# Performance work log

Hardware: AMD Instinct MI355X
Metric: run time of the kernel (lower is better)

The kernel has to match this reference:

```python
import jax, jax.numpy as jnp
import numpy as np
import math

# ---------------- irreps configuration (mul, l, parity) ----------------
MUL = 32
IRREPS_IN1 = [(MUL, 0, 1), (MUL, 1, -1), (MUL, 2, 1)]   # 32x0e + 32x1o + 32x2e
IRREPS_IN2 = [(1, 0, 1), (1, 1, -1), (1, 2, 1)]          # 1x0e + 1x1o + 1x2e (edge spherical harmonics)
IRREPS_OUT = [(MUL, 0, 1), (MUL, 1, -1), (MUL, 2, 1)]
BATCH = 8192

def _dim(irreps):
    return sum(mul * (2 * l + 1) for mul, l, _ in irreps)

# ---------------- real Wigner-3j tensors (e3nn convention) ----------------
def _su2_cg_coeff(j1, m1, j2, m2, j3, m3):
    if m3 != m1 + m2:
        return 0.0
    f = math.factorial
    vmin = max(-j1 + j2 + m3, -j1 + m1, 0)
    vmax = min(j2 + j3 + m1, j3 - j1 + j2, j3 + m3)
    C = math.sqrt((2 * j3 + 1) * f(j3 + j1 - j2) * f(j3 - j1 + j2) * f(j1 + j2 - j3)
                  * f(j3 + m3) * f(j3 - m3)
                  / (f(j1 + j2 + j3 + 1) * f(j1 - m1) * f(j1 + m1) * f(j2 - m2) * f(j2 + m2)))
    S = 0.0
    for v in range(vmin, vmax + 1):
        S += (-1.0) ** (v + j2 + m2) * f(j2 + j3 + m1 - v) * f(j1 - m1 + v) / (
            f(v) * f(j3 - j1 + j2 - v) * f(j3 + m3 - v) * f(v + j1 - j2 - m3))
    return C * S

def _su2_cg(l1, l2, l3):
    m = np.zeros((2 * l1 + 1, 2 * l2 + 1, 2 * l3 + 1))
    for m1 in range(-l1, l1 + 1):
        for m2 in range(-l2, l2 + 1):
            m3 = m1 + m2
            if abs(m3) <= l3:
                m[l1 + m1, l2 + m2, l3 + m3] = _su2_cg_coeff(l1, m1, l2, m2, l3, m3)
    return m / math.sqrt(2 * l3 + 1)  # 3j normalization -> Frobenius norm 1

def _q(l):
    # change of basis real -> complex spherical harmonics, with (-i)^l phase to make 3j real
    q = np.zeros((2 * l + 1, 2 * l + 1), dtype=np.complex128)
    for m in range(-l, 0):
        q[l + m, l + abs(m)] = 1 / math.sqrt(2)
        q[l + m, l - abs(m)] = -1j / math.sqrt(2)
    q[l, l] = 1.0
    for m in range(1, l + 1):
        q[l + m, l + abs(m)] = (-1) ** m / math.sqrt(2)
        q[l + m, l - abs(m)] = 1j * (-1) ** m / math.sqrt(2)
    return (-1j) ** l * q

def _w3j(l1, l2, l3):
    Ccplx = _su2_cg(l1, l2, l3).astype(np.complex128)
    Q1, Q2, Q3 = _q(l1), _q(l2), _q(l3)
    C = np.einsum('ij,kl,mn,ikm->jln', Q1, Q2, np.conj(Q3), Ccplx)
    if np.abs(C.imag).max() > 1e-8:  # robust fallback for basis-direction convention
        C = np.einsum('ji,lk,nm,ikm->jln', np.conj(Q1), np.conj(Q2), Q3, Ccplx)
    return np.real(C).astype(np.float32)

W3J = {}
for _m1, l1, _p1 in IRREPS_IN1:
    for _m2, l2, _p2 in IRREPS_IN2:
        for l3 in range(abs(l1 - l2), l1 + l2 + 1):
            if (l1, l2, l3) not in W3J:
                W3J[(l1, l2, l3)] = _w3j(l1, l2, l3)

# ---------------- tp output structure and linear weight layout ----------------
def _tp_irreps_out():
    irr = []
    for mul1, l1, p1 in IRREPS_IN1:
        for mul2, l2, p2 in IRREPS_IN2:
            for l3 in range(abs(l1 - l2), l1 + l2 + 1):
                irr.append((mul1 * mul2, l3, p1 * p2))
    return irr

TP_IRREPS = _tp_irreps_out()
WEIGHT_NUMEL = sum(mul_out * sum(m for m, li, pi in TP_IRREPS if (li, pi) == (l, p))
                   for mul_out, l, p in IRREPS_OUT)  # = 11264

# ---------------- forward ----------------
def _full_tp(x, y):
    # x: [B, 288], y: [B, 9] -> z: [B, 2592], 15 CG paths, 'uvuv' mode, component norm
    segs = []
    off1 = 0
    for mul1, l1, p1 in IRREPS_IN1:
        d1 = 2 * l1 + 1
        x1 = x[:, off1:off1 + mul1 * d1].reshape(-1, mul1, d1)
        off1 += mul1 * d1
        off2 = 0
        for mul2, l2, p2 in IRREPS_IN2:
            d2 = 2 * l2 + 1
            x2 = y[:, off2:off2 + mul2 * d2].reshape(-1, mul2, d2)
            off2 += mul2 * d2
            for l3 in range(abs(l1 - l2), l1 + l2 + 1):
                C = jnp.asarray(W3J[(l1, l2, l3)])
                z = jnp.einsum('ijk,bui,bvj->buvk', C, x1, x2) * np.float32(math.sqrt(2 * l3 + 1))
                segs.append(z.reshape(z.shape[0], -1))
    return jnp.concatenate(segs, axis=1)

def _linear(z, weight):
    # e3nn o3.Linear with external per-sample weights, element path normalization
    zsegs, off = [], 0
    for mul, l, p in TP_IRREPS:
        d = 2 * l + 1
        zsegs.append((z[:, off:off + mul * d].reshape(-1, mul, d), l, p))
        off += mul * d
    outs, woff = [], 0
    for mul_out, l, p in IRREPS_OUT:
        xin = jnp.concatenate([s for s, li, pi in zsegs if (li, pi) == (l, p)], axis=1)  # [B, U, d]
        U = xin.shape[1]
        w = weight[:, woff:woff + U * mul_out].reshape(-1, U, mul_out)
        woff += U * mul_out
        o = jnp.einsum('bud,buo->bod', xin, w) * np.float32(1.0 / math.sqrt(U))
        outs.append(o.reshape(o.shape[0], -1))
    return jnp.concatenate(outs, axis=1)

def setup_inputs() -> dict:
    key = jax.random.key(0)
    k1, k2, k3 = jax.random.split(key, 3)
    x = jax.random.normal(k1, (BATCH, _dim(IRREPS_IN1)), dtype=jnp.float32)
    y = jax.random.normal(k2, (BATCH, _dim(IRREPS_IN2)), dtype=jnp.float32)
    weight = jax.random.normal(k3, (BATCH, WEIGHT_NUMEL), dtype=jnp.float32)
    return {"x": x, "y": y, "weight": weight}

def reference(x, y, weight):
    z = _full_tp(x, y)
    return _linear(z, weight)
```

## Files before the change

### kernel.cpp

```cpp
#include <hip/hip_runtime.h>


using f4 = float __attribute__((ext_vector_type(4)));

__device__ inline f4 wred8(f4 v) {
#pragma unroll
    for (int m = 8; m <= 32; m <<= 1) {
        v.x += __shfl_xor(v.x, m);
        v.y += __shfl_xor(v.y, m);
        v.z += __shfl_xor(v.z, m);
        v.w += __shfl_xor(v.w, m);
    }
    return v;
}

__global__ __launch_bounds__(256) void etp_fused(
    const float* __restrict__ xg,
    const float* __restrict__ yg,
    const float* __restrict__ wg,
    float* __restrict__ outg)
{
    const int b = blockIdx.x;
    const int t = threadIdx.x;

    __shared__ __align__(16) float xs[288];
    __shared__ float ys[9];
    __shared__ float z0s[96];
    __shared__ float z1s[384];
    __shared__ float z2s[640];
    __shared__ float red[288 * 5];

    if (t < 72) {
        reinterpret_cast<f4*>(xs)[t] =
            __builtin_nontemporal_load(reinterpret_cast<const f4*>(xg) + (size_t)b * 72 + t);
    } else if (t < 81) {
        ys[t - 72] = yg[(size_t)b * 9 + (t - 72)];
    }

    const int oq = t & 7;
    const int ug = t >> 3;
    const f4* w4 = reinterpret_cast<const f4*>(wg) + (size_t)b * 2816;

    f4 wa0 = __builtin_nontemporal_load(&w4[(0 * 32 + ug) * 8 + oq]);
    f4 wa1 = __builtin_nontemporal_load(&w4[(1 * 32 + ug) * 8 + oq]);
    f4 wa2 = __builtin_nontemporal_load(&w4[(2 * 32 + ug) * 8 + oq]);
    f4 wb0 = __builtin_nontemporal_load(&w4[768 + (0 * 32 + ug) * 8 + oq]);
    f4 wb1 = __builtin_nontemporal_load(&w4[768 + (1 * 32 + ug) * 8 + oq]);
    f4 wb2 = __builtin_nontemporal_load(&w4[768 + (2 * 32 + ug) * 8 + oq]);
    f4 wb3 = __builtin_nontemporal_load(&w4[768 + (3 * 32 + ug) * 8 + oq]);
    f4 wc0 = __builtin_nontemporal_load(&w4[1792 + (0 * 32 + ug) * 8 + oq]);
    f4 wc1 = __builtin_nontemporal_load(&w4[1792 + (1 * 32 + ug) * 8 + oq]);
    f4 wc2 = __builtin_nontemporal_load(&w4[1792 + (2 * 32 + ug) * 8 + oq]);
    f4 wc3 = __builtin_nontemporal_load(&w4[1792 + (3 * 32 + ug) * 8 + oq]);

    __syncthreads();

    const float y0 = ys[0];
    const float ya = ys[1], yb = ys[2], yc = ys[3];
    const float Y0 = ys[4], Y1 = ys[5], Y2 = ys[6], Y3 = ys[7], Y4 = ys[8];

    constexpr float S3  = 0.5477225575051661f;
    constexpr float D3  = 0.31622776601683794f;
    constexpr float TD3 = 0.6324555320336759f;
    constexpr float S5  = 0.7071067811865476f;
    constexpr float D5  = 0.4082482904638631f;
    constexpr float P5  = 0.5345224838248488f;
    constexpr float Q5  = 0.2672612419124244f;
    constexpr float R5  = 0.4629100498862757f;
    constexpr float N3  = 0.5773502691896258f;
    constexpr float N5  = 0.4472135954999579f;

    if (t < 128) {
        const int u = t;
        float o0, o1, o2;
        if (u < 32) {
            const float s = xs[u];
            o0 = s * ya; o1 = s * yb; o2 = s * yc;
        } else if (u < 64) {
            const float* p = &xs[32 + 3 * (u - 32)];
            o0 = p[0] * y0; o1 = p[1] * y0; o2 = p[2] * y0;
        } else if (u < 96) {
            const float* p = &xs[32 + 3 * (u - 64)];
            const float a = p[0], bz = p[1], cx = p[2];
            o0 = S3 * (cx * Y0 + bz * Y1 - a * Y4) - D3 * a * Y2;
            o1 = S3 * (a * Y1 + cx * Y3) + TD3 * bz * Y2;
            o2 = S3 * (a * Y0 + bz * Y3 + cx * Y4) - D3 * cx * Y2;
        } else {
            const float* p = &xs[128 + 5 * (u - 96)];
            const float X0 = p[0], X1 = p[1], X2 = p[2], X3 = p[3], X4 = p[4];
            o0 = S3 * (yc * X0 + yb * X1 - ya * X4) - D3 * ya * X2;
            o1 = S3 * (ya * X1 + yc * X3) + TD3 * yb * X2;
            o2 = S3 * (ya * X0 + yb * X3 + yc * X4) - D3 * yc * X2;
        }
        z1s[3 * u] = o0; z1s[3 * u + 1] = o1; z1s[3 * u + 2] = o2;
    } else {
        const int u = t - 128;
        float c0, c1, c2, c3, c4;
        if (u < 32) {
            const float s = xs[u];
            c0 = s * Y0; c1 = s * Y1; c2 = s * Y2; c3 = s * Y3; c4 = s * Y4;
        } else if (u < 64) {
            const float* p = &xs[32 + 3 * (u - 32)];
            const float a = p[0], bz = p[1], cx = p[2];
            c0 = S5 * (a * yc + cx * ya);
            c1 = S5 * (a * yb + bz * ya);
            c2 = D5 * (2.0f * bz * yb - a * ya - cx * yc);
            c3 = S5 * (cx * yb + bz * yc);
            c4 = S5 * (cx * yc - a * ya);
        } else if (u < 96) {
            const float* p = &xs[128 + 5 * (u - 64)];
            c0 = p[0] * y0; c1 = p[1] * y0; c2 = p[2] * y0; c3 = p[3] * y0; c4 = p[4] * y0;
        } else {
            const float* p = &xs[128 + 5 * (u - 96)];
            const float X0 = p[0], X1 = p[1], X2 = p[2], X3 = p[3], X4 = p[4];
            c0 = -P5 * (X0 * Y2 + X2 * Y0) + R5 * (X1 * Y3 + X3 * Y1);
            c1 =  Q5 * (X1 * Y2 + X2 * Y1) - R5 * (X1 * Y4 + X4 * Y1) + R5 * (X0 * Y3 + X3 * Y0);
            c2 =  P5 * (X2 * Y2 - X0 * Y0 - X4 * Y4) + Q5 * (X1 * Y1 + X3 * Y3);
            c3 =  Q5 * (X3 * Y2 + X2 * Y3) + R5 * (X3 * Y4 + X4 * Y3) + R5 * (X0 * Y1 + X1 * Y0);
            c4 = -P5 * (X4 * Y2 + X2 * Y4) + R5 * (X3 * Y3 - X1 * Y1);
        }
        float* zp = &z2s[5 * u];
        zp[0] = c0; zp[1] = c1; zp[2] = c2; zp[3] = c3; zp[4] = c4;
    }
    if (t < 96) {
        float v;
        if (t < 32) {
            v = xs[t] * y0;
        } else if (t < 64) {
            const float* p = &xs[32 + 3 * (t - 32)];
            v = N3 * (p[0] * ya + p[1] * yb + p[2] * yc);
        } else {
            const float* p = &xs[128 + 5 * (t - 64)];
            v = N5 * (p[0] * Y0 + p[1] * Y1 + p[2] * Y2 + p[3] * Y3 + p[4] * Y4);
        }
        z0s[t] = v;
    }
    __syncthreads();

    f4 a0   = wa0 * z0s[ug] + wa1 * z0s[32 + ug] + wa2 * z0s[64 + ug];

    f4 a1k0 = {0,0,0,0}, a1k1 = {0,0,0,0}, a1k2 = {0,0,0,0};
    {
        const f4 w0 = wb0, w1 = wb1, w2 = wb2, w3 = wb3;
        const int u0 = ug, u1 = 32 + ug, u2 = 64 + ug, u3 = 96 + ug;
        a1k0 = w0 * z1s[3*u0]   + w1 * z1s[3*u1]   + w2 * z1s[3*u2]   + w3 * z1s[3*u3];
        a1k1 = w0 * z1s[3*u0+1] + w1 * z1s[3*u1+1] + w2 * z1s[3*u2+1] + w3 * z1s[3*u3+1];
        a1k2 = w0 * z1s[3*u0+2] + w1 * z1s[3*u1+2] + w2 * z1s[3*u2+2] + w3 * z1s[3*u3+2];
    }
    f4 a2k0, a2k1, a2k2, a2k3, a2k4;
    {
        const f4 w0 = wc0, w1 = wc1, w2 = wc2, w3 = wc3;
        const int u0 = ug, u1 = 32 + ug, u2 = 64 + ug, u3 = 96 + ug;
        a2k0 = w0 * z2s[5*u0]   + w1 * z2s[5*u1]   + w2 * z2s[5*u2]   + w3 * z2s[5*u3];
        a2k1 = w0 * z2s[5*u0+1] + w1 * z2s[5*u1+1] + w2 * z2s[5*u2+1] + w3 * z2s[5*u3+1];
        a2k2 = w0 * z2s[5*u0+2] + w1 * z2s[5*u1+2] + w2 * z2s[5*u2+2] + w3 * z2s[5*u3+2];
        a2k3 = w0 * z2s[5*u0+3] + w1 * z2s[5*u1+3] + w2 * z2s[5*u2+3] + w3 * z2s[5*u3+3];
        a2k4 = w0 * z2s[5*u0+4] + w1 * z2s[5*u1+4] + w2 * z2s[5*u2+4] + w3 * z2s[5*u3+4];
    }

    a0   = wred8(a0);
    a1k0 = wred8(a1k0); a1k1 = wred8(a1k1); a1k2 = wred8(a1k2);
    a2k0 = wred8(a2k0); a2k1 = wred8(a2k1); a2k2 = wred8(a2k2);
    a2k3 = wred8(a2k3); a2k4 = wred8(a2k4);

    const int lane = t & 63;
    const int wv   = t >> 6;
    if ((lane >> 3) == 0) {
        const int o = lane * 4;
#pragma unroll
        for (int j = 0; j < 4; ++j) {
            red[(o + j) * 5 + wv]                       = a0[j];
            red[(32 + (o + j) * 3 + 0) * 5 + wv]        = a1k0[j];
            red[(32 + (o + j) * 3 + 1) * 5 + wv]        = a1k1[j];
            red[(32 + (o + j) * 3 + 2) * 5 + wv]        = a1k2[j];
            red[(128 + (o + j) * 5 + 0) * 5 + wv]       = a2k0[j];
            red[(128 + (o + j) * 5 + 1) * 5 + wv]       = a2k1[j];
            red[(128 + (o + j) * 5 + 2) * 5 + wv]       = a2k2[j];
            red[(128 + (o + j) * 5 + 3) * 5 + wv]       = a2k3[j];
            red[(128 + (o + j) * 5 + 4) * 5 + wv]       = a2k4[j];
        }
    }
    __syncthreads();

    if (t < 72) {
        const float scale = (t < 8) ? 0.10206207261596575f
                                    : 0.08838834764831845f;
        f4 r;
#pragma unroll
        for (int j = 0; j < 4; ++j) {
            const int idx = 4 * t + j;
            r[j] = (red[idx * 5 + 0] + red[idx * 5 + 1] +
                    red[idx * 5 + 2] + red[idx * 5 + 3]) * scale;
        }
        __builtin_nontemporal_store(r, reinterpret_cast<f4*>(outg) + (size_t)b * 72 + t);
    }
}

extern "C" void kernel_launch(void* const* d_in, const int* in_sizes, int n_in,
                              void* d_out, int out_size, void* d_ws, size_t ws_size,
                              hipStream_t stream) {
    const float* x = (const float*)d_in[0];
    const float* y = (const float*)d_in[1];
    const float* w = (const float*)d_in[2];
    float* out = (float*)d_out;
    const int rows = in_sizes[0] / 288;
    etp_fused<<<rows, 256, 0, stream>>>(x, y, w, out);
}
```

Baseline: 65.10 us.

## Process four rows per block with register prefetch of next row's inputs

Each block now loops over four consecutive batch rows instead of one. It issues the next row's x, y and weight loads into registers right after the current row's weights have been consumed, so global memory latency overlaps with the contraction and reduction work. The grid shrinks by four, which cuts block launch and setup overhead. In exchange there are fewer resident blocks to hide latency, each iteration serializes more barriers, and register pressure rises.

After: 74.46 us. 14.4% more time.

```diff
diff --git a/kernel.cpp b/kernel.cpp
--- a/kernel.cpp
+++ b/kernel.cpp
@@ -2,6 +2,8 @@
 
 
 using f4 = float __attribute__((ext_vector_type(4)));
+
+#define ROWS 4
 
 __device__ inline f4 wred8(f4 v) {
 #pragma unroll
@@ -18,10 +20,11 @@
     const float* __restrict__ xg,
     const float* __restrict__ yg,
     const float* __restrict__ wg,
-    float* __restrict__ outg)
+    float* __restrict__ outg,
+    int nrows)
 {
-    const int b = blockIdx.x;
     const int t = threadIdx.x;
+    const int row0 = blockIdx.x * ROWS;
 
     __shared__ __align__(16) float xs[288];
     __shared__ float ys[9];
@@ -30,34 +33,46 @@
     __shared__ float z2s[640];
     __shared__ float red[288 * 5];
 
-    if (t < 72) {
-        reinterpret_cast<f4*>(xs)[t] =
-            __builtin_nontemporal_load(reinterpret_cast<const f4*>(xg) + (size_t)b * 72 + t);
-    } else if (t < 81) {
-        ys[t - 72] = yg[(size_t)b * 9 + (t - 72)];
-    }
-
     const int oq = t & 7;
     const int ug = t >> 3;
-    const f4* w4 = reinterpret_cast<const f4*>(wg) + (size_t)b * 2816;
-
-    f4 wa0 = __builtin_nontemporal_load(&w4[(0 * 32 + ug) * 8 + oq]);
-    f4 wa1 = __builtin_nontemporal_load(&w4[(1 * 32 + ug) * 8 + oq]);
-    f4 wa2 = __builtin_nontemporal_load(&w4[(2 * 32 + ug) * 8 + oq]);
-    f4 wb0 = __builtin_nontemporal_load(&w4[768 + (0 * 32 + ug) * 8 + oq]);
-    f4 wb1 = __builtin_nontemporal_load(&w4[768 + (1 * 32 + ug) * 8 + oq]);
-    f4 wb2 = __builtin_nontemporal_load(&w4[768 + (2 * 32 + ug) * 8 + oq]);
-    f4 wb3 = __builtin_nontemporal_load(&w4[768 + (3 * 32 + ug) * 8 + oq]);
-    f4 wc0 = __builtin_nontemporal_load(&w4[1792 + (0 * 32 + ug) * 8 + oq]);
-    f4 wc1 = __builtin_nontemporal_load(&w4[1792 + (1 * 32 + ug) * 8 + oq]);
-    f4 wc2 = __builtin_nontemporal_load(&w4[1792 + (2 * 32 + ug) * 8 + oq]);
-    f4 wc3 = __builtin_nontemporal_load(&w4[1792 + (3 * 32 + ug) * 8 + oq]);
-
-    __syncthreads();
-
-    const float y0 = ys[0];
-    const float ya = ys[1], yb = ys[2], yc = ys[3];
-    const float Y0 = ys[4], Y1 = ys[5], Y2 = ys[6], Y3 = ys[7], Y4 = ys[8];
+    const f4* xg4 = reinterpret_cast<const f4*>(xg);
+
+    f4 xv = {0, 0, 0, 0};
+    float yv = 0.f;
+    f4 wa0, wa1, wa2, wb0, wb1, wb2, wb3, wc0, wc1, wc2, wc3;
+
+    auto issue_xy = [&](int r) {
+        if (t < 72) {
+            xv = __builtin_nontemporal_load(&xg4[(size_t)r * 72 + t]);
+        } else if (t < 81) {
+            yv = yg[(size_t)r * 9 + (t - 72)];
+        }
+    };
+    auto issue_wa = [&](int r) {
+        const f4* w4 = reinterpret_cast<const f4*>(wg) + (size_t)r * 2816;
+        wa0 = __builtin_nontemporal_load(&w4[(0 * 32 + ug) * 8 + oq]);
+        wa1 = __builtin_nontemporal_load(&w4[(1 * 32 + ug) * 8 + oq]);
+        wa2 = __builtin_nontemporal_load(&w4[(2 * 32 + ug) * 8 + oq]);
+    };
+    auto issue_wb = [&](int r) {
+        const f4* w4 = reinterpret_cast<const f4*>(wg) + (size_t)r * 2816;
+        wb0 = __builtin_nontemporal_load(&w4[768 + (0 * 32 + ug) * 8 + oq]);
+        wb1 = __builtin_nontemporal_load(&w4[768 + (1 * 32 + ug) * 8 + oq]);
+        wb2 = __builtin_nontemporal_load(&w4[768 + (2 * 32 + ug) * 8 + oq]);
+        wb3 = __builtin_nontemporal_load(&w4[768 + (3 * 32 + ug) * 8 + oq]);
+    };
+    auto issue_wc = [&](int r) {
+        const f4* w4 = reinterpret_cast<const f4*>(wg) + (size_t)r * 2816;
+        wc0 = __builtin_nontemporal_load(&w4[1792 + (0 * 32 + ug) * 8 + oq]);
+        wc1 = __builtin_nontemporal_load(&w4[1792 + (1 * 32 + ug) * 8 + oq]);
+        wc2 = __builtin_nontemporal_load(&w4[1792 + (2 * 32 + ug) * 8 + oq]);
+        wc3 = __builtin_nontemporal_load(&w4[1792 + (3 * 32 + ug) * 8 + oq]);
+    };
+
+    issue_xy(row0);
+    issue_wa(row0);
+    issue_wb(row0);
+    issue_wc(row0);
 
     constexpr float S3  = 0.5477225575051661f;
     constexpr float D3  = 0.31622776601683794f;
@@ -70,129 +85,156 @@
     constexpr float N3  = 0.5773502691896258f;
     constexpr float N5  = 0.4472135954999579f;
 
-    if (t < 128) {
-        const int u = t;
-        float o0, o1, o2;
-        if (u < 32) {
-            const float s = xs[u];
-            o0 = s * ya; o1 = s * yb; o2 = s * yc;
-        } else if (u < 64) {
-            const float* p = &xs[32 + 3 * (u - 32)];
-            o0 = p[0] * y0; o1 = p[1] * y0; o2 = p[2] * y0;
-        } else if (u < 96) {
-            const float* p = &xs[32 + 3 * (u - 64)];
-            const float a = p[0], bz = p[1], cx = p[2];
-            o0 = S3 * (cx * Y0 + bz * Y1 - a * Y4) - D3 * a * Y2;
-            o1 = S3 * (a * Y1 + cx * Y3) + TD3 * bz * Y2;
-            o2 = S3 * (a * Y0 + bz * Y3 + cx * Y4) - D3 * cx * Y2;
+    for (int rr = 0; rr < ROWS; ++rr) {
+        const int r = row0 + rr;
+        if (r >= nrows) break;
+        const bool more = (rr + 1 < ROWS) && (r + 1 < nrows);
+
+        if (t < 72) {
+            reinterpret_cast<f4*>(xs)[t] = xv;
+        } else if (t < 81) {
+            ys[t - 72] = yv;
+        }
+        __syncthreads();
+
+        const float y0 = ys[0];
+        const float ya = ys[1], yb = ys[2], yc = ys[3];
+        const float Y0 = ys[4], Y1 = ys[5], Y2 = ys[6], Y3 = ys[7], Y4 = ys[8];
+
+        if (t < 128) {
+            const int u = t;
+            float o0, o1, o2;
+            if (u < 32) {
+                const float s = xs[u];
+                o0 = s * ya; o1 = s * yb; o2 = s * yc;
+            } else if (u < 64) {
+                const float* p = &xs[32 + 3 * (u - 32)];
+                o0 = p[0] * y0; o1 = p[1] * y0; o2 = p[2] * y0;
+            } else if (u < 96) {
+                const float* p = &xs[32 + 3 * (u - 64)];
+                const float a = p[0], bz = p[1], cx = p[2];
+                o0 = S3 * (cx * Y0 + bz * Y1 - a * Y4) - D3 * a * Y2;
+                o1 = S3 * (a * Y1 + cx * Y3) + TD3 * bz * Y2;
+                o2 = S3 * (a * Y0 + bz * Y3 + cx * Y4) - D3 * cx * Y2;
+            } else {
+                const float* p = &xs[128 + 5 * (u - 96)];
+                const float X0 = p[0], X1 = p[1], X2 = p[2], X3 = p[3], X4 = p[4];
+                o0 = S3 * (yc * X0 + yb * X1 - ya * X4) - D3 * ya * X2;
+                o1 = S3 * (ya * X1 + yc * X3) + TD3 * yb * X2;
+                o2 = S3 * (ya * X0 + yb * X3 + yc * X4) - D3 * yc * X2;
+            }
+            z1s[3 * u] = o0; z1s[3 * u + 1] = o1; z1s[3 * u + 2] = o2;
         } else {
-            const float* p = &xs[128 + 5 * (u - 96)];
-            const float X0 = p[0], X1 = p[1], X2 = p[2], X3 = p[3], X4 = p[4];
-            o0 = S3 * (yc * X0 + yb * X1 - ya * X4) - D3 * ya * X2;
-            o1 = S3 * (ya * X1 + yc * X3) + TD3 * yb * X2;
-            o2 = S3 * (ya * X0 + yb * X3 + yc * X4) - D3 * yc * X2;
-        }
-        z1s[3 * u] = o0; z1s[3 * u + 1] = o1; z1s[3 * u + 2] = o2;
-    } else {
-        const int u = t - 128;
-        float c0, c1, c2, c3, c4;
-        if (u < 32) {
-            const float s = xs[u];
-            c0 = s * Y0; c1 = s * Y1; c2 = s * Y2; c3 = s * Y3; c4 = s * Y4;
-        } else if (u < 64) {
-            const float* p = &xs[32 + 3 * (u - 32)];
-            const float a = p[0], bz = p[1], cx = p[2];
-            c0 = S5 * (a * yc + cx * ya);
-            c1 = S5 * (a * yb + bz * ya);
-            c2 = D5 * (2.0f * bz * yb - a * ya - cx * yc);
-            c3 = S5 * (cx * yb + bz * yc);
-            c4 = S5 * (cx * yc - a * ya);
-        } else if (u < 96) {
-            const float* p = &xs[128 + 5 * (u - 64)];
-            c0 = p[0] * y0; c1 = p[1] * y0; c2 = p[2] * y0; c3 = p[3] * y0; c4 = p[4] * y0;
-        } else {
-            const float* p = &xs[128 + 5 * (u - 96)];
-            const float X0 = p[0], X1 = p[1], X2 = p[2], X3 = p[3], X4 = p[4];
-            c0 = -P5 * (X0 * Y2 + X2 * Y0) + R5 * (X1 * Y3 + X3 * Y1);
-            c1 =  Q5 * (X1 * Y2 + X2 * Y1) - R5 * (X1 * Y4 + X4 * Y1) + R5 * (X0 * Y3 + X3 * Y0);
-            c2 =  P5 * (X2 * Y2 - X0 * Y0 - X4 * Y4) + Q5 * (X1 * Y1 + X3 * Y3);
-            c3 =  Q5 * (X3 * Y2 + X2 * Y3) + R5 * (X3 * Y4 + X4 * Y3) + R5 * (X0 * Y1 + X1 * Y0);
-            c4 = -P5 * (X4 * Y2 + X2 * Y4) + R5 * (X3 * Y3 - X1 * Y1);
-        }
-        float* zp = &z2s[5 * u];
-        zp[0] = c0; zp[1] = c1; zp[2] = c2; zp[3] = c3; zp[4] = c4;
-    }
-    if (t < 96) {
-        float v;
-        if (t < 32) {
-            v = xs[t] * y0;
-        } else if (t < 64) {
-            const float* p = &xs[32 + 3 * (t - 32)];
-            v = N3 * (p[0] * ya + p[1] * yb + p[2] * yc);
-        } else {
-            const float* p = &xs[128 + 5 * (t - 64)];
-            v = N5 * (p[0] * Y0 + p[1] * Y1 + p[2] * Y2 + p[3] * Y3 + p[4] * Y4);
-        }
-        z0s[t] = v;
-    }
-    __syncthreads();
-
-    f4 a0   = wa0 * z0s[ug] + wa1 * z0s[32 + ug] + wa2 * z0s[64 + ug];
-
-    f4 a1k0 = {0,0,0,0}, a1k1 = {0,0,0,0}, a1k2 = {0,0,0,0};
-    {
-        const f4 w0 = wb0, w1 = wb1, w2 = wb2, w3 = wb3;
+            const int u = t - 128;
+            float c0, c1, c2, c3, c4;
+            if (u < 32) {
+                const float s = xs[u];
+                c0 = s * Y0; c1 = s * Y1; c2 = s * Y2; c3 = s * Y3; c4 = s * Y4;
+            } else if (u < 64) {
+                const float* p = &xs[32 + 3 * (u - 32)];
+                const float a = p[0], bz = p[1], cx = p[2];
+                c0 = S5 * (a * yc + cx * ya);
+                c1 = S5 * (a * yb + bz * ya);
+                c2 = D5 * (2.0f * bz * yb - a * ya - cx * yc);
+                c3 = S5 * (cx * yb + bz * yc);
+                c4 = S5 * (cx * yc - a * ya);
+            } else if (u < 96) {
+                const float* p = &xs[128 + 5 * (u - 64)];
+                c0 = p[0] * y0; c1 = p[1] * y0; c2 = p[2] * y0; c3 = p[3] * y0; c4 = p[4] * y0;
+            } else {
+                const float* p = &xs[128 + 5 * (u - 96)];
+                const float X0 = p[0], X1 = p[1], X2 = p[2], X3 = p[3], X4 = p[4];
+                c0 = -P5 * (X0 * Y2 + X2 * Y0) + R5 * (X1 * Y3 + X3 * Y1);
+                c1 =  Q5 * (X1 * Y2 + X2 * Y1) - R5 * (X1 * Y4 + X4 * Y1) + R5 * (X0 * Y3 + X3 * Y0);
+                c2 =  P5 * (X2 * Y2 - X0 * Y0 - X4 * Y4) + Q5 * (X1 * Y1 + X3 * Y3);
+                c3 =  Q5 * (X3 * Y2 + X2 * Y3) + R5 * (X3 * Y4 + X4 * Y3) + R5 * (X0 * Y1 + X1 * Y0);
+                c4 = -P5 * (X4 * Y2 + X2 * Y4) + R5 * (X3 * Y3 - X1 * Y1);
+            }
+            float* zp = &z2s[5 * u];
+            zp[0] = c0; zp[1] = c1; zp[2] = c2; zp[3] = c3; zp[4] = c4;
+        }
+        if (t < 96) {
+            float v;
+            if (t < 32) {
+                v = xs[t] * y0;
+            } else if (t < 64) {
+                const float* p = &xs[32 + 3 * (t - 32)];
+                v = N3 * (p[0] * ya + p[1] * yb + p[2] * yc);
+            } else {
+                const float* p = &xs[128 + 5 * (t - 64)];
+                v = N5 * (p[0] * Y0 + p[1] * Y1 + p[2] * Y2 + p[3] * Y3 + p[4] * Y4);
+            }
+            z0s[t] = v;
+        }
+        __syncthreads();
+
+        const int lane = t & 63;
+        const int wv   = t >> 6;
         const int u0 = ug, u1 = 32 + ug, u2 = 64 + ug, u3 = 96 + ug;
-        a1k0 = w0 * z1s[3*u0]   + w1 * z1s[3*u1]   + w2 * z1s[3*u2]   + w3 * z1s[3*u3];
-        a1k1 = w0 * z1s[3*u0+1] + w1 * z1s[3*u1+1] + w2 * z1s[3*u2+1] + w3 * z1s[3*u3+1];
-        a1k2 = w0 * z1s[3*u0+2] + w1 * z1s[3*u1+2] + w2 * z1s[3*u2+2] + w3 * z1s[3*u3+2];
-    }
-    f4 a2k0, a2k1, a2k2, a2k3, a2k4;
-    {
-        const f4 w0 = wc0, w1 = wc1, w2 = wc2, w3 = wc3;
-        const int u0 = ug, u1 = 32 + ug, u2 = 64 + ug, u3 = 96 + ug;
-        a2k0 = w0 * z2s[5*u0]   + w1 * z2s[5*u1]   + w2 * z2s[5*u2]   + w3 * z2s[5*u3];
-        a2k1 = w0 * z2s[5*u0+1] + w1 * z2s[5*u1+1] + w2 * z2s[5*u2+1] + w3 * z2s[5*u3+1];
-        a2k2 = w0 * z2s[5*u0+2] + w1 * z2s[5*u1+2] + w2 * z2s[5*u2+2] + w3 * z2s[5*u3+2];
-        a2k3 = w0 * z2s[5*u0+3] + w1 * z2s[5*u1+3] + w2 * z2s[5*u2+3] + w3 * z2s[5*u3+3];
-        a2k4 = w0 * z2s[5*u0+4] + w1 * z2s[5*u1+4] + w2 * z2s[5*u2+4] + w3 * z2s[5*u3+4];
-    }
-
-    a0   = wred8(a0);
-    a1k0 = wred8(a1k0); a1k1 = wred8(a1k1); a1k2 = wred8(a1k2);
-    a2k0 = wred8(a2k0); a2k1 = wred8(a2k1); a2k2 = wred8(a2k2);
-    a2k3 = wred8(a2k3); a2k4 = wred8(a2k4);
-
-    const int lane = t & 63;
-    const int wv   = t >> 6;
-    if ((lane >> 3) == 0) {
-        const int o = lane * 4;
-#pragma unroll
-        for (int j = 0; j < 4; ++j) {
-            red[(o + j) * 5 + wv]                       = a0[j];
-            red[(32 + (o + j) * 3 + 0) * 5 + wv]        = a1k0[j];
-            red[(32 + (o + j) * 3 + 1) * 5 + wv]        = a1k1[j];
-            red[(32 + (o + j) * 3 + 2) * 5 + wv]        = a1k2[j];
-            red[(128 + (o + j) * 5 + 0) * 5 + wv]       = a2k0[j];
-            red[(128 + (o + j) * 5 + 1) * 5 + wv]       = a2k1[j];
-            red[(128 + (o + j) * 5 + 2) * 5 + wv]       = a2k2[j];
-            red[(128 + (o + j) * 5 + 3) * 5 + wv]       = a2k3[j];
-            red[(128 + (o + j) * 5 + 4) * 5 + wv]       = a2k4[j];
-        }
-    }
-    __syncthreads();
-
-    if (t < 72) {
-        const float scale = (t < 8) ? 0.10206207261596575f
-                                    : 0.08838834764831845f;
-        f4 r;
-#pragma unroll
-        for (int j = 0; j < 4; ++j) {
-            const int idx = 4 * t + j;
-            r[j] = (red[idx * 5 + 0] + red[idx * 5 + 1] +
-                    red[idx * 5 + 2] + red[idx * 5 + 3]) * scale;
-        }
-        __builtin_nontemporal_store(r, reinterpret_cast<f4*>(outg) + (size_t)b * 72 + t);
+
+        if (more) issue_xy(r + 1);
+
+        {
+            f4 a0 = wa0 * z0s[u0] + wa1 * z0s[u1] + wa2 * z0s[u2];
+            if (more) issue_wa(r + 1);
+            a0 = wred8(a0);
+            if (lane < 8) {
+                const int o = lane * 4;
+#pragma unroll
+                for (int j = 0; j < 4; ++j) red[(o + j) * 5 + wv] = a0[j];
+            }
+        }
+        {
+            f4 a1k0 = wb0 * z1s[3*u0]   + wb1 * z1s[3*u1]   + wb2 * z1s[3*u2]   + wb3 * z1s[3*u3];
+            f4 a1k1 = wb0 * z1s[3*u0+1] + wb1 * z1s[3*u1+1] + wb2 * z1s[3*u2+1] + wb3 * z1s[3*u3+1];
+            f4 a1k2 = wb0 * z1s[3*u0+2] + wb1 * z1s[3*u1+2] + wb2 * z1s[3*u2+2] + wb3 * z1s[3*u3+2];
+            if (more) issue_wb(r + 1);
+            a1k0 = wred8(a1k0); a1k1 = wred8(a1k1); a1k2 = wred8(a1k2);
+            if (lane < 8) {
+                const int o = lane * 4;
+#pragma unroll
+                for (int j = 0; j < 4; ++j) {
+                    red[(32 + (o + j) * 3 + 0) * 5 + wv] = a1k0[j];
+                    red[(32 + (o + j) * 3 + 1) * 5 + wv] = a1k1[j];
+                    red[(32 + (o + j) * 3 + 2) * 5 + wv] = a1k2[j];
+                }
+            }
+        }
+        {
+            f4 a2k0 = wc0 * z2s[5*u0]   + wc1 * z2s[5*u1]   + wc2 * z2s[5*u2]   + wc3 * z2s[5*u3];
+            f4 a2k1 = wc0 * z2s[5*u0+1] + wc1 * z2s[5*u1+1] + wc2 * z2s[5*u2+1] + wc3 * z2s[5*u3+1];
+            f4 a2k2 = wc0 * z2s[5*u0+2] + wc1 * z2s[5*u1+2] + wc2 * z2s[5*u2+2] + wc3 * z2s[5*u3+2];
+            f4 a2k3 = wc0 * z2s[5*u0+3] + wc1 * z2s[5*u1+3] + wc2 * z2s[5*u2+3] + wc3 * z2s[5*u3+3];
+            f4 a2k4 = wc0 * z2s[5*u0+4] + wc1 * z2s[5*u1+4] + wc2 * z2s[5*u2+4] + wc3 * z2s[5*u3+4];
+            if (more) issue_wc(r + 1);
+            a2k0 = wred8(a2k0); a2k1 = wred8(a2k1); a2k2 = wred8(a2k2);
+            a2k3 = wred8(a2k3); a2k4 = wred8(a2k4);
+            if (lane < 8) {
+                const int o = lane * 4;
+#pragma unroll
+                for (int j = 0; j < 4; ++j) {
+                    red[(128 + (o + j) * 5 + 0) * 5 + wv] = a2k0[j];
+                    red[(128 + (o + j) * 5 + 1) * 5 + wv] = a2k1[j];
+                    red[(128 + (o + j) * 5 + 2) * 5 + wv] = a2k2[j];
+                    red[(128 + (o + j) * 5 + 3) * 5 + wv] = a2k3[j];
+                    red[(128 + (o + j) * 5 + 4) * 5 + wv] = a2k4[j];
+                }
+            }
+        }
+        __syncthreads();
+
+        if (t < 72) {
+            const float scale = (t < 8) ? 0.10206207261596575f
+                                        : 0.08838834764831845f;
+            f4 res;
+#pragma unroll
+            for (int j = 0; j < 4; ++j) {
+                const int idx = 4 * t + j;
+                res[j] = (red[idx * 5 + 0] + red[idx * 5 + 1] +
+                          red[idx * 5 + 2] + red[idx * 5 + 3]) * scale;
+            }
+            __builtin_nontemporal_store(res, reinterpret_cast<f4*>(outg) + (size_t)r * 72 + t);
+        }
     }
 }
 
@@ -203,6 +245,7 @@
     const float* y = (const float*)d_in[1];
     const float* w = (const float*)d_in[2];
     float* out = (float*)d_out;
-    const int rows = in_sizes[0] / 288;
-    etp_fused<<<rows, 256, 0, stream>>>(x, y, w, out);
+    const int nrows = in_sizes[0] / 288;
+    const int grid = (nrows + ROWS - 1) / ROWS;
+    etp_fused<<<grid, 256, 0, stream>>>(x, y, w, out, nrows);
 }
```
